# Performance work log

Hardware: AMD Instinct MI355X
Metric: run time of the kernel (lower is better)

## Reference

```python
import jax, jax.numpy as jnp
import numpy as np

B, S, D, H, F = 2, 2048, 1024, 16, 4096
HD = D // H
EPS = 1e-5


def _layernorm(x, g, b):
    mu = jnp.mean(x, axis=-1, keepdims=True)
    var = jnp.var(x, axis=-1, keepdims=True)
    return (x - mu) * jax.lax.rsqrt(var + EPS) * g + b


def setup_inputs() -> dict:
    key = jax.random.key(0)
    ks = jax.random.split(key, 10)
    sd = 0.02
    return {
        "src": jax.random.normal(ks[0], (B, S, D), jnp.float32),
        "qkv_w": jax.random.normal(ks[1], (3 * D, D), jnp.float32) * sd,
        "qkv_b": jnp.zeros((3 * D,), jnp.float32),
        "out_w": jax.random.normal(ks[2], (D, D), jnp.float32) * sd,
        "out_b": jnp.zeros((D,), jnp.float32),
        "ffn_w1": jax.random.normal(ks[3], (F, D), jnp.float32) * sd,
        "ffn_b1": jnp.zeros((F,), jnp.float32),
        "ffn_w2": jax.random.normal(ks[4], (D, F), jnp.float32) * sd,
        "ffn_b2": jnp.zeros((D,), jnp.float32),
        "ln1_g": jnp.ones((D,), jnp.float32),
        "ln1_b": jnp.zeros((D,), jnp.float32),
        "ln2_g": jnp.ones((D,), jnp.float32),
        "ln2_b": jnp.zeros((D,), jnp.float32),
    }


def reference(src, qkv_w, qkv_b, out_w, out_b, ffn_w1, ffn_b1, ffn_w2, ffn_b2,
              ln1_g, ln1_b, ln2_g, ln2_b):
    # --- Multi-head self-attention (post-norm, dropout=identity in eval) ---
    qkv = src @ qkv_w.T + qkv_b                        # [B,S,3D]
    qkv = qkv.reshape(B, S, H, 3 * HD).transpose(0, 2, 1, 3)  # [B,H,S,3hd]
    q, k, v = jnp.split(qkv, 3, axis=-1)               # each [B,H,S,hd]
    scores = jnp.einsum('bhqd,bhkd->bhqk', q, k) / np.sqrt(HD).astype(np.float32)
    attn = jax.nn.softmax(scores, axis=-1)
    ctx = jnp.einsum('bhqk,bhkd->bhqd', attn, v)       # [B,H,S,hd]
    ctx = ctx.transpose(0, 2, 1, 3).reshape(B, S, D)
    mha_out = ctx @ out_w.T + out_b
    agg = _layernorm(src + mha_out, ln1_g, ln1_b)
    # --- FFN: Linear -> ReLU -> Linear ---
    h = jax.nn.relu(agg @ ffn_w1.T + ffn_b1)
    ffn_out = h @ ffn_w2.T + ffn_b2
    return _layernorm(agg + ffn_out, ln2_g, ln2_b)
```

## Files before the change

### kernel.cpp

```cpp
#include <hip/hip_runtime.h>


typedef unsigned short u16;
typedef unsigned int u32;
typedef __attribute__((ext_vector_type(8))) __bf16 bf16x8;
typedef __attribute__((ext_vector_type(4))) float f32x4;
typedef __attribute__((ext_vector_type(4))) short s16x4;
typedef __attribute__((ext_vector_type(2))) u32 u32x2;

__device__ __forceinline__ u16 f2bf(float f) {
  u32 u = __float_as_uint(f);
  u += 0x7fffu + ((u >> 16) & 1u);
  return (u16)(u >> 16);
}

__device__ __forceinline__ float bf2f(u16 h) {
  return __uint_as_float((u32)h << 16);
}

__device__ __forceinline__ u32 pk_bf_trunc(float a, float b) {
  return (__float_as_uint(a) >> 16) | (__float_as_uint(b) & 0xffff0000u);
}

__device__ __forceinline__ float exp2_fast(float x) {
  float t = __builtin_fmaf(x, 8388608.0f, 1064992506.0f);
  return __int_as_float((int)t);
}

__device__ __forceinline__ void async16(const void* g, void* l) {
  __builtin_amdgcn_global_load_lds((__attribute__((address_space(1))) void*)g,
                                   (__attribute__((address_space(3))) void*)l,
                                   16, 0, 0);
}

__device__ __forceinline__ f32x4 mfma16(bf16x8 a, bf16x8 b, f32x4 c) {
  return __builtin_amdgcn_mfma_f32_16x16x32_bf16(a, b, c, 0, 0, 0);
}

__device__ __forceinline__ f32x4 mfma_pv(s16x4 a, s16x4 b, f32x4 c) {
#if __has_builtin(__builtin_amdgcn_mfma_f32_16x16x16bf16_1k)
  return __builtin_amdgcn_mfma_f32_16x16x16bf16_1k(a, b, c, 0, 0, 0);
#else
  f32x4 d;
  asm("v_mfma_f32_16x16x16_bf16 %0, %1, %2, %3" : "=v"(d) : "v"(a), "v"(b), "v"(c));
  return d;
#endif
}

__global__ __launch_bounds__(256)
void cvt_all(const float* __restrict__ qkv_w, const float* __restrict__ out_w,
             const float* __restrict__ f1, const float* __restrict__ f2,
             const float* __restrict__ src,
             u16* __restrict__ o_qkv, u16* __restrict__ o_out,
             u16* __restrict__ o_f1, u16* __restrict__ o_f2,
             u16* __restrict__ o_src) {
  int b = blockIdx.x;
  const float* in;
  u16* out;
  int lb, ob;
  if (b < 3072) {
    int h = b / 192, c = b - h * 192;
    ob = (c < 64) ? h * 64 + c : (c < 128) ? 1024 + h * 64 + (c - 64)
                                           : 2048 + h * 64 + (c - 128);
    in = qkv_w; out = o_qkv; lb = b;
  }
  else if (b < 4096)  { in = out_w; out = o_out; lb = b - 3072;  ob = lb; }
  else if (b < 8192)  { in = f1;    out = o_f1;  lb = b - 4096;  ob = lb; }
  else if (b < 12288) { in = f2;    out = o_f2;  lb = b - 8192;  ob = lb; }
  else                { in = src;   out = o_src; lb = b - 12288; ob = lb; }
  int i = lb * 256 + threadIdx.x;
  int o = ob * 256 + threadIdx.x;
  float4 v = ((const float4*)in)[i];
  ushort4 ov;
  ov.x = f2bf(v.x); ov.y = f2bf(v.y); ov.z = f2bf(v.z); ov.w = f2bf(v.w);
  ((ushort4*)out)[o] = ov;
}

template <int MODE, int SPLIT>
__global__ __launch_bounds__(256)
void gemm_bt(const u16* __restrict__ A, const u16* __restrict__ W,
             const float* __restrict__ bias,
             u16* __restrict__ outb,
             u16* __restrict__ qo, u16* __restrict__ ko, u16* __restrict__ vto,
             int M, int N, int K) {
  __shared__ u16 As[128 * 64];
  __shared__ u16 Bs[128 * 64];
  const int lane = threadIdx.x & 63;
  const int wave = threadIdx.x >> 6;
  const int lrow = lane & 15;
  const int lq = lane >> 4;
  const int tm = blockIdx.x * 128;
  const int tn = blockIdx.y * 128;
  const int wm = (wave >> 1) * 64;
  const int wn = (wave & 1) * 64;
  const int kc = K / SPLIT;
  const int kbeg = blockIdx.z * kc;
  f32x4 acc[4][4] = {};

  for (int k0 = kbeg; k0 < kbeg + kc; k0 += 64) {
#pragma unroll
    for (int c = 0; c < 4; ++c) {
      int chunk = wave * 256 + c * 64 + lane;
      int row = chunk >> 3;
      int sc = chunk & 7;
      int cc = sc ^ (row & 7);
      u16* la = As + (size_t)(wave * 256 + c * 64) * 8;
      u16* lb = Bs + (size_t)(wave * 256 + c * 64) * 8;
      async16(A + (size_t)(tm + row) * K + (k0 + cc * 8), la);
      async16(W + (size_t)(tn + row) * K + (k0 + cc * 8), lb);
    }
    __syncthreads();
#pragma unroll
    for (int h = 0; h < 2; ++h) {
      bf16x8 a_frag[4], b_frag[4];
#pragma unroll
      for (int i = 0; i < 4; ++i) {
        int row = wm + i * 16 + lrow;
        int sc = (h * 4 + lq) ^ (row & 7);
        a_frag[i] = *(const bf16x8*)(As + row * 64 + sc * 8);
      }
#pragma unroll
      for (int j = 0; j < 4; ++j) {
        int row = wn + j * 16 + lrow;
        int sc = (h * 4 + lq) ^ (row & 7);
        b_frag[j] = *(const bf16x8*)(Bs + row * 64 + sc * 8);
      }
#pragma unroll
      for (int i = 0; i < 4; ++i)
#pragma unroll
        for (int j = 0; j < 4; ++j)
          acc[i][j] = mfma16(a_frag[i], b_frag[j], acc[i][j]);
    }
    __syncthreads();
  }

  if constexpr (MODE == 2) {
    const int type = tn >> 10;
    if (type < 2) {
      u16* dst = (type == 0) ? qo : ko;
      const float scale = (type == 0) ? 0.1803368801f : 1.f;
#pragma unroll
      for (int j = 0; j < 4; ++j) {
        int idx = (tn & 1023) + wn + j * 16 + lrow;
        int hh = idx >> 6, c = idx & 63;
        float bv = bias[hh * 192 + type * 64 + c];
#pragma unroll
        for (int i = 0; i < 4; ++i) {
#pragma unroll
          for (int r = 0; r < 4; ++r) {
            int row = tm + wm + i * 16 + lq * 4 + r;
            int b = row >> 11, s = row & 2047;
            dst[(((size_t)(b * 16 + hh) * 2048 + s) << 6) + c] =
                f2bf((acc[i][j][r] + bv) * scale);
          }
        }
      }
    } else {
#pragma unroll
      for (int j = 0; j < 4; ++j) {
        int idx = (tn & 1023) + wn + j * 16 + lrow;
        int hh = idx >> 6, c = idx & 63;
        float bv = bias[hh * 192 + 128 + c];
#pragma unroll
        for (int i = 0; i < 4; ++i) {
          int row0 = tm + wm + i * 16 + lq * 4;
          int b = row0 >> 11, s0 = row0 & 2047;
          ushort4 pk;
          pk.x = f2bf(acc[i][j][0] + bv);
          pk.y = f2bf(acc[i][j][1] + bv);
          pk.z = f2bf(acc[i][j][2] + bv);
          pk.w = f2bf(acc[i][j][3] + bv);
          *(ushort4*)(vto + (((size_t)(b * 16 + hh) * 64 + c) << 11) + s0) = pk;
        }
      }
    }
    return;
  }

  u16* outp = outb;
  if constexpr (MODE == 0) outp += (size_t)blockIdx.z * M * N;

#pragma unroll
  for (int i = 0; i < 4; ++i) {
#pragma unroll
    for (int j = 0; j < 4; ++j) {
      int col = tn + wn + j * 16 + lrow;
      float bv = (SPLIT == 1 || blockIdx.z == 0) ? bias[col] : 0.f;
#pragma unroll
      for (int r = 0; r < 4; ++r) {
        int row = tm + wm + i * 16 + lq * 4 + r;
        float v = acc[i][j][r] + bv;
        if constexpr (MODE == 0) {
          outp[(size_t)row * N + col] = f2bf(v);
        } else {
          outp[(size_t)row * N + col] = f2bf(fmaxf(v, 0.f));
        }
      }
    }
  }
}

__global__ __launch_bounds__(512)
void attn_kernel(const u16* __restrict__ Q, const u16* __restrict__ K,
                 const u16* __restrict__ Vt,
                 u16* __restrict__ o_part, float* __restrict__ l_part) {
  __shared__ u16 Ks[128 * 64];
  __shared__ u16 Vs[64 * 128];
  const int tid = threadIdx.x;
  const int lane = tid & 63;
  const int wave = tid >> 6;
  const int wq = wave & 3;
  const int role = wave >> 2;
  const int lrow = lane & 15;
  const int q = lane >> 4;
  const int bh = blockIdx.x & 31;
  const int qb = (blockIdx.x >> 5) & 7;
  const int kvh = blockIdx.x >> 8;
  const u16* Qp = Q + ((size_t)bh * 2048 + qb * 256) * 64;
  const u16* Kp = K + (size_t)bh * 2048 * 64;
  const u16* Vp = Vt + (size_t)bh * 64 * 2048;

  bf16x8 qf[2][2];
#pragma unroll
  for (int h2 = 0; h2 < 2; ++h2)
#pragma unroll
    for (int kk = 0; kk < 2; ++kk)
      qf[h2][kk] = *(const bf16x8*)(Qp + (h2 * 128 + wave * 16 + lrow) * 64 +
                                    kk * 32 + q * 8);

  const s16x4 ones = {(short)0x3F80, (short)0x3F80, (short)0x3F80, (short)0x3F80};
  f32x4 oacc[2][4] = {};
  f32x4 lacc[2] = {};

  for (int kb = kvh * 8; kb < kvh * 8 + 8; ++kb) {
    if (role == 0) {
#pragma unroll
      for (int t = 0; t < 4; ++t) {
        int c = wq * 256 + t * 64 + lane;
        int row = c >> 3, sc = c & 7;
        int cc = sc ^ (row & 7);
        async16(Kp + (size_t)(kb * 128 + row) * 64 + cc * 8,
                Ks + (size_t)(wq * 256 + t * 64) * 8);
      }
    } else {
#pragma unroll
      for (int t = 0; t < 4; ++t) {
        int c = wq * 256 + t * 64 + lane;
        int row = c >> 4, sc = c & 15;
        int cc = sc ^ (row & 7);
        async16(Vp + (size_t)row * 2048 + kb * 128 + cc * 8,
                Vs + (size_t)(wq * 256 + t * 64) * 8);
      }
    }
    __syncthreads();

#pragma unroll
    for (int h2 = 0; h2 < 2; ++h2) {
      f32x4 sacc[8] = {};
#pragma unroll
      for (int j = 0; j < 8; ++j) {
#pragma unroll
        for (int kk = 0; kk < 2; ++kk) {
          int row = j * 16 + lrow;
          int sc = (kk * 4 + q) ^ (row & 7);
          bf16x8 kf = *(const bf16x8*)(Ks + row * 64 + sc * 8);
          sacc[j] = mfma16(kf, qf[h2][kk], sacc[j]);
        }
      }

      s16x4 pa[8];
#pragma unroll
      for (int j = 0; j < 8; ++j) {
        float p0 = exp2_fast(sacc[j][0]);
        float p1 = exp2_fast(sacc[j][1]);
        float p2 = exp2_fast(sacc[j][2]);
        float p3 = exp2_fast(sacc[j][3]);
        u32x2 pw;
        pw.x = pk_bf_trunc(p0, p1);
        pw.y = pk_bf_trunc(p2, p3);
        pa[j] = __builtin_bit_cast(s16x4, pw);
      }

#pragma unroll
      for (int j = 0; j < 8; ++j) {
        lacc[h2] = mfma_pv(pa[j], ones, lacc[h2]);
#pragma unroll
        for (int jn = 0; jn < 4; ++jn) {
          int row = jn * 16 + lrow;
          int sc = (j * 2 + (q >> 1)) ^ (row & 7);
          s16x4 vb = *(const s16x4*)(Vs + row * 128 + sc * 8 + (q & 1) * 4);
          oacc[h2][jn] = mfma_pv(pa[j], vb, oacc[h2][jn]);
        }
      }
    }
    __syncthreads();
  }

  const int b = bh >> 4, h = bh & 15;
  u16* op = o_part + (size_t)kvh * 4096 * 1024;
  float* lp = l_part + kvh * 65536 + bh * 2048;
#pragma unroll
  for (int h2 = 0; h2 < 2; ++h2) {
#pragma unroll
    for (int r = 0; r < 4; ++r) {
      int s = qb * 256 + h2 * 128 + wave * 16 + q * 4 + r;
      if (lrow == 0) lp[s] = lacc[h2][r];
      size_t base = ((size_t)(b * 2048 + s)) * 1024 + h * 64;
#pragma unroll
      for (int jn = 0; jn < 4; ++jn)
        op[base + jn * 16 + lrow] = f2bf(oacc[h2][jn][r]);
    }
  }
}

__global__ __launch_bounds__(256)
void attn_combine(const u16* __restrict__ o_part, const float* __restrict__ l_part,
                  u16* __restrict__ ctx) {
  const int t = blockIdx.x;
  const int tid = threadIdx.x;
  __shared__ float linv[16];
  if (tid < 16) {
    int b = t >> 11, s = t & 2047;
    int bh = b * 16 + tid;
    linv[tid] = 1.f / (l_part[bh * 2048 + s] + l_part[65536 + bh * 2048 + s]);
  }
  __syncthreads();
  size_t base = (size_t)t * 1024;
  ushort4 a = ((const ushort4*)(o_part + base))[tid];
  ushort4 c = ((const ushort4*)(o_part + 4096ull * 1024 + base))[tid];
  float li = linv[tid >> 4];
  ushort4 o;
  o.x = f2bf((bf2f(a.x) + bf2f(c.x)) * li);
  o.y = f2bf((bf2f(a.y) + bf2f(c.y)) * li);
  o.z = f2bf((bf2f(a.z) + bf2f(c.z)) * li);
  o.w = f2bf((bf2f(a.w) + bf2f(c.w)) * li);
  ((ushort4*)(ctx + base))[tid] = o;
}

template <int P>
__global__ __launch_bounds__(256)
void ln_kernel(const float* __restrict__ x1, const u16* __restrict__ x2,
               const float* __restrict__ g, const float* __restrict__ bb,
               float* __restrict__ outf, u16* __restrict__ outb) {
  const int t = blockIdx.x;
  const int tid = threadIdx.x;
  const int lane = tid & 63, wave = tid >> 6;
  const size_t base = (size_t)t * 1024;
  const size_t pstride = 4096ull * 1024;
  float v[4];
  float s = 0.f, s2 = 0.f;
#pragma unroll
  for (int e = 0; e < 4; ++e) {
    int i = tid + e * 256;
    float x = x1[base + i];
#pragma unroll
    for (int p = 0; p < P; ++p) x += bf2f(x2[p * pstride + base + i]);
    v[e] = x;
    s += x;
    s2 += x * x;
  }
#pragma unroll
  for (int d = 1; d < 64; d <<= 1) {
    s += __shfl_xor(s, d);
    s2 += __shfl_xor(s2, d);
  }
  __shared__ float red[8];
  if (lane == 0) { red[wave] = s; red[4 + wave] = s2; }
  __syncthreads();
  s = red[0] + red[1] + red[2] + red[3];
  s2 = red[4] + red[5] + red[6] + red[7];
  float mean = s * (1.f / 1024.f);
  float var = s2 * (1.f / 1024.f) - mean * mean;
  float rstd = rsqrtf(var + 1e-5f);
#pragma unroll
  for (int e = 0; e < 4; ++e) {
    int i = tid + e * 256;
    float y = (v[e] - mean) * rstd * g[i] + bb[i];
    outf[base + i] = y;
    if (outb) outb[base + i] = f2bf(y);
  }
}

extern "C" void kernel_launch(void* const* d_in, const int* in_sizes, int n_in,
                              void* d_out, int out_size, void* d_ws, size_t ws_size,
                              hipStream_t stream) {
  const float* src    = (const float*)d_in[0];
  const float* qkv_w  = (const float*)d_in[1];
  const float* qkv_b  = (const float*)d_in[2];
  const float* out_w  = (const float*)d_in[3];
  const float* out_b  = (const float*)d_in[4];
  const float* ffn_w1 = (const float*)d_in[5];
  const float* ffn_b1 = (const float*)d_in[6];
  const float* ffn_w2 = (const float*)d_in[7];
  const float* ffn_b2 = (const float*)d_in[8];
  const float* ln1_g  = (const float*)d_in[9];
  const float* ln1_b  = (const float*)d_in[10];
  const float* ln2_g  = (const float*)d_in[11];
  const float* ln2_b  = (const float*)d_in[12];

  char* ws = (char*)d_ws;
  size_t off = 0;
  auto alloc = [&](size_t bytes) -> void* {
    void* p = ws + off;
    off += (bytes + 255) & ~(size_t)255;
    return p;
  };
  u16* wqkv = (u16*)alloc(3072ull * 1024 * 2);
  u16* wout = (u16*)alloc(1024ull * 1024 * 2);
  u16* wf1  = (u16*)alloc(4096ull * 1024 * 2);
  u16* wf2  = (u16*)alloc(1024ull * 4096 * 2);
  u16* srcb = (u16*)alloc(4096ull * 1024 * 2);
  u16* qb_  = (u16*)alloc(32ull * 2048 * 64 * 2);
  u16* kb_  = (u16*)alloc(32ull * 2048 * 64 * 2);
  u16* vtb  = (u16*)alloc(32ull * 64 * 2048 * 2);
  u16* opart = (u16*)alloc(2ull * 4096 * 1024 * 2);
  float* lpart = (float*)alloc(2ull * 65536 * 4);
  u16* ctxb = (u16*)alloc(4096ull * 1024 * 2);
  u16* mha  = (u16*)alloc(4ull * 4096 * 1024 * 2);
  float* aggf = (float*)alloc(4096ull * 1024 * 4);
  u16* aggb = (u16*)alloc(4096ull * 1024 * 2);
  u16* hb   = (u16*)alloc(4096ull * 4096 * 2);
  u16* ffnf = (u16*)alloc(4ull * 4096 * 1024 * 2);

  cvt_all<<<16384, 256, 0, stream>>>(qkv_w, out_w, ffn_w1, ffn_w2, src,
                                     wqkv, wout, wf1, wf2, srcb);

  gemm_bt<2, 1><<<dim3(32, 24), 256, 0, stream>>>(srcb, wqkv, qkv_b, nullptr,
                                                  qb_, kb_, vtb, 4096, 3072, 1024);
  attn_kernel<<<512, 512, 0, stream>>>(qb_, kb_, vtb, opart, lpart);
  attn_combine<<<4096, 256, 0, stream>>>(opart, lpart, ctxb);
  gemm_bt<0, 4><<<dim3(32, 8, 4), 256, 0, stream>>>(ctxb, wout, out_b, mha,
                                                    nullptr, nullptr, nullptr, 4096, 1024, 1024);
  ln_kernel<4><<<4096, 256, 0, stream>>>(src, mha, ln1_g, ln1_b, aggf, aggb);
  gemm_bt<1, 1><<<dim3(32, 32), 256, 0, stream>>>(aggb, wf1, ffn_b1, hb,
                                                  nullptr, nullptr, nullptr, 4096, 4096, 1024);
  gemm_bt<0, 4><<<dim3(32, 8, 4), 256, 0, stream>>>(hb, wf2, ffn_b2, ffnf,
                                                    nullptr, nullptr, nullptr, 4096, 1024, 4096);
  ln_kernel<4><<<4096, 256, 0, stream>>>(aggf, ffnf, ln2_g, ln2_b, (float*)d_out, nullptr);
}
```

Baseline: 382.8 us.

## Add 256x256-tile 8-wave ping-pong GEMM for QKV and FFN1 projections

Adds a new GEMM kernel with 256x256 output tiles, 8 waves, and 128KB dynamic LDS holding double-buffered A/B tiles. Its main loop interleaves async global-to-LDS staging with quarter-tile MFMA phases under barriers and s_setprio, so loads overlap compute. The QKV projection (with its head-split Q/K/V^T epilogue moved over) and the FFN1 ReLU GEMM now use it with XCD-aware block swizzling, replacing the 128x128 kernel. The trade-off is high register and LDS pressure with few workgroups: 192 and 256 blocks respectively.

Result: faster. 374.7 us (-2.1%).

```diff
diff --git a/kernel.cpp b/kernel.cpp
--- a/kernel.cpp
+++ b/kernel.cpp
@@ -134,49 +134,6 @@
     __syncthreads();
   }
 
-  if constexpr (MODE == 2) {
-    const int type = tn >> 10;
-    if (type < 2) {
-      u16* dst = (type == 0) ? qo : ko;
-      const float scale = (type == 0) ? 0.1803368801f : 1.f;
-#pragma unroll
-      for (int j = 0; j < 4; ++j) {
-        int idx = (tn & 1023) + wn + j * 16 + lrow;
-        int hh = idx >> 6, c = idx & 63;
-        float bv = bias[hh * 192 + type * 64 + c];
-#pragma unroll
-        for (int i = 0; i < 4; ++i) {
-#pragma unroll
-          for (int r = 0; r < 4; ++r) {
-            int row = tm + wm + i * 16 + lq * 4 + r;
-            int b = row >> 11, s = row & 2047;
-            dst[(((size_t)(b * 16 + hh) * 2048 + s) << 6) + c] =
-                f2bf((acc[i][j][r] + bv) * scale);
-          }
-        }
-      }
-    } else {
-#pragma unroll
-      for (int j = 0; j < 4; ++j) {
-        int idx = (tn & 1023) + wn + j * 16 + lrow;
-        int hh = idx >> 6, c = idx & 63;
-        float bv = bias[hh * 192 + 128 + c];
-#pragma unroll
-        for (int i = 0; i < 4; ++i) {
-          int row0 = tm + wm + i * 16 + lq * 4;
-          int b = row0 >> 11, s0 = row0 & 2047;
-          ushort4 pk;
-          pk.x = f2bf(acc[i][j][0] + bv);
-          pk.y = f2bf(acc[i][j][1] + bv);
-          pk.z = f2bf(acc[i][j][2] + bv);
-          pk.w = f2bf(acc[i][j][3] + bv);
-          *(ushort4*)(vto + (((size_t)(b * 16 + hh) * 64 + c) << 11) + s0) = pk;
-        }
-      }
-    }
-    return;
-  }
-
   u16* outp = outb;
   if constexpr (MODE == 0) outp += (size_t)blockIdx.z * M * N;
 
@@ -194,6 +151,257 @@
           outp[(size_t)row * N + col] = f2bf(v);
         } else {
           outp[(size_t)row * N + col] = f2bf(fmaxf(v, 0.f));
+        }
+      }
+    }
+  }
+}
+
+template <int MODE>
+__global__ __launch_bounds__(512, 2)
+void gemm8p(const u16* __restrict__ A, const u16* __restrict__ W,
+            const float* __restrict__ bias, u16* __restrict__ outb,
+            u16* __restrict__ qo, u16* __restrict__ ko, u16* __restrict__ vto,
+            int N) {
+  extern __shared__ u16 lds[];
+  constexpr int K = 1024;
+  constexpr int NTK = K / 64;
+  constexpr int NG = NTK / 2;
+  u16* As = lds;
+  u16* Bs = lds + 32768;
+  const int tid = threadIdx.x;
+  const int lane = tid & 63;
+  const int wave = tid >> 6;
+  const int lrow = lane & 15;
+  const int lq = lane >> 4;
+  const int wm = wave >> 2;
+  const int wn = wave & 3;
+
+  const int nwg = gridDim.x;
+  const int wg = blockIdx.x;
+  const int swz = (wg & 7) * (nwg >> 3) + (wg >> 3);
+  const int tm = (swz & 15) * 256;
+  const int tn = (swz >> 4) * 256;
+
+  auto stage = [&](const u16* __restrict__ T, int trow0, int kt, int rbase,
+                   u16* base) {
+#pragma unroll
+    for (int it = 0; it < 2; ++it) {
+      int c = it * 512 + tid;
+      int row = c >> 3, sc = c & 7, cc = sc ^ (row & 7);
+      async16(T + (size_t)(trow0 + rbase + row) * K + kt * 64 + cc * 8,
+              base + rbase * 64 + (it * 512 + wave * 64) * 8);
+    }
+  };
+  auto ldA = [&](int buf, int m, int h) {
+    int row = wm * 128 + m * 16 + lrow;
+    int sc = (h * 4 + lq) ^ (row & 7);
+    return *(const bf16x8*)(As + buf * 16384 + row * 64 + sc * 8);
+  };
+  auto ldB = [&](int buf, int n, int h) {
+    int row = wn * 64 + n * 16 + lrow;
+    int sc = (h * 4 + lq) ^ (row & 7);
+    return *(const bf16x8*)(Bs + buf * 16384 + row * 64 + sc * 8);
+  };
+
+  f32x4 acc[8][4] = {};
+  bf16x8 a[4][2], b[4][2];
+
+  stage(A, tm, 0, 0, As);
+  stage(A, tm, 0, 128, As);
+  stage(W, tn, 0, 0, Bs);
+  stage(W, tn, 0, 128, Bs);
+  stage(W, tn, 1, 0, Bs + 16384);
+  stage(A, tm, 1, 0, As + 16384);
+  asm volatile("s_waitcnt vmcnt(4)" ::: "memory");
+  __builtin_amdgcn_s_barrier();
+
+  for (int g = 0; g < NG; ++g) {
+    const int t = 2 * g;
+    const int t1k = t + 1;
+    const int t2k = (t + 2 < NTK) ? t + 2 : NTK - 1;
+    const int t3k = (t + 3 < NTK) ? t + 3 : NTK - 1;
+
+#pragma unroll
+    for (int m = 0; m < 4; ++m) { a[m][0] = ldA(0, m, 0); a[m][1] = ldA(0, m, 1); }
+#pragma unroll
+    for (int n = 0; n < 2; ++n) { b[n][0] = ldB(0, n, 0); b[n][1] = ldB(0, n, 1); }
+    stage(A, tm, t1k, 128, As + 16384);
+    __builtin_amdgcn_s_barrier();
+    asm volatile("s_waitcnt lgkmcnt(0)" ::: "memory");
+    __builtin_amdgcn_s_setprio(1);
+#pragma unroll
+    for (int m = 0; m < 4; ++m)
+#pragma unroll
+      for (int n = 0; n < 2; ++n) {
+        acc[m][n] = mfma16(a[m][0], b[n][0], acc[m][n]);
+        acc[m][n] = mfma16(a[m][1], b[n][1], acc[m][n]);
+      }
+    __builtin_amdgcn_s_setprio(0);
+    __builtin_amdgcn_s_barrier();
+
+#pragma unroll
+    for (int n = 0; n < 2; ++n) { b[2 + n][0] = ldB(0, 2 + n, 0); b[2 + n][1] = ldB(0, 2 + n, 1); }
+    stage(W, tn, t1k, 128, Bs + 16384);
+    __builtin_amdgcn_s_barrier();
+    asm volatile("s_waitcnt lgkmcnt(0)" ::: "memory");
+    __builtin_amdgcn_s_setprio(1);
+#pragma unroll
+    for (int m = 0; m < 4; ++m)
+#pragma unroll
+      for (int n = 0; n < 2; ++n) {
+        acc[m][2 + n] = mfma16(a[m][0], b[2 + n][0], acc[m][2 + n]);
+        acc[m][2 + n] = mfma16(a[m][1], b[2 + n][1], acc[m][2 + n]);
+      }
+    __builtin_amdgcn_s_setprio(0);
+    __builtin_amdgcn_s_barrier();
+
+#pragma unroll
+    for (int m = 0; m < 4; ++m) { a[m][0] = ldA(0, 4 + m, 0); a[m][1] = ldA(0, 4 + m, 1); }
+    stage(W, tn, t2k, 0, Bs);
+    __builtin_amdgcn_s_barrier();
+    asm volatile("s_waitcnt lgkmcnt(0)" ::: "memory");
+    __builtin_amdgcn_s_setprio(1);
+#pragma unroll
+    for (int m = 0; m < 4; ++m)
+#pragma unroll
+      for (int n = 0; n < 2; ++n) {
+        acc[4 + m][n] = mfma16(a[m][0], b[n][0], acc[4 + m][n]);
+        acc[4 + m][n] = mfma16(a[m][1], b[n][1], acc[4 + m][n]);
+      }
+    __builtin_amdgcn_s_setprio(0);
+    __builtin_amdgcn_s_barrier();
+
+    stage(A, tm, t2k, 0, As);
+    asm volatile("s_waitcnt vmcnt(4)" ::: "memory");
+    __builtin_amdgcn_s_barrier();
+    __builtin_amdgcn_s_setprio(1);
+#pragma unroll
+    for (int m = 0; m < 4; ++m)
+#pragma unroll
+      for (int n = 0; n < 2; ++n) {
+        acc[4 + m][2 + n] = mfma16(a[m][0], b[2 + n][0], acc[4 + m][2 + n]);
+        acc[4 + m][2 + n] = mfma16(a[m][1], b[2 + n][1], acc[4 + m][2 + n]);
+      }
+    __builtin_amdgcn_s_setprio(0);
+    __builtin_amdgcn_s_barrier();
+
+#pragma unroll
+    for (int m = 0; m < 4; ++m) { a[m][0] = ldA(1, m, 0); a[m][1] = ldA(1, m, 1); }
+#pragma unroll
+    for (int n = 0; n < 2; ++n) { b[n][0] = ldB(1, n, 0); b[n][1] = ldB(1, n, 1); }
+    stage(A, tm, t2k, 128, As);
+    __builtin_amdgcn_s_barrier();
+    asm volatile("s_waitcnt lgkmcnt(0)" ::: "memory");
+    __builtin_amdgcn_s_setprio(1);
+#pragma unroll
+    for (int m = 0; m < 4; ++m)
+#pragma unroll
+      for (int n = 0; n < 2; ++n) {
+        acc[m][n] = mfma16(a[m][0], b[n][0], acc[m][n]);
+        acc[m][n] = mfma16(a[m][1], b[n][1], acc[m][n]);
+      }
+    __builtin_amdgcn_s_setprio(0);
+    __builtin_amdgcn_s_barrier();
+
+#pragma unroll
+    for (int n = 0; n < 2; ++n) { b[2 + n][0] = ldB(1, 2 + n, 0); b[2 + n][1] = ldB(1, 2 + n, 1); }
+    stage(W, tn, t2k, 128, Bs);
+    __builtin_amdgcn_s_barrier();
+    asm volatile("s_waitcnt lgkmcnt(0)" ::: "memory");
+    __builtin_amdgcn_s_setprio(1);
+#pragma unroll
+    for (int m = 0; m < 4; ++m)
+#pragma unroll
+      for (int n = 0; n < 2; ++n) {
+        acc[m][2 + n] = mfma16(a[m][0], b[2 + n][0], acc[m][2 + n]);
+        acc[m][2 + n] = mfma16(a[m][1], b[2 + n][1], acc[m][2 + n]);
+      }
+    __builtin_amdgcn_s_setprio(0);
+    __builtin_amdgcn_s_barrier();
+
+#pragma unroll
+    for (int m = 0; m < 4; ++m) { a[m][0] = ldA(1, 4 + m, 0); a[m][1] = ldA(1, 4 + m, 1); }
+    stage(W, tn, t3k, 0, Bs + 16384);
+    __builtin_amdgcn_s_barrier();
+    asm volatile("s_waitcnt lgkmcnt(0)" ::: "memory");
+    __builtin_amdgcn_s_setprio(1);
+#pragma unroll
+    for (int m = 0; m < 4; ++m)
+#pragma unroll
+      for (int n = 0; n < 2; ++n) {
+        acc[4 + m][n] = mfma16(a[m][0], b[n][0], acc[4 + m][n]);
+        acc[4 + m][n] = mfma16(a[m][1], b[n][1], acc[4 + m][n]);
+      }
+    __builtin_amdgcn_s_setprio(0);
+    __builtin_amdgcn_s_barrier();
+
+    stage(A, tm, t3k, 0, As + 16384);
+    asm volatile("s_waitcnt vmcnt(4)" ::: "memory");
+    __builtin_amdgcn_s_barrier();
+    __builtin_amdgcn_s_setprio(1);
+#pragma unroll
+    for (int m = 0; m < 4; ++m)
+#pragma unroll
+      for (int n = 0; n < 2; ++n) {
+        acc[4 + m][2 + n] = mfma16(a[m][0], b[2 + n][0], acc[4 + m][2 + n]);
+        acc[4 + m][2 + n] = mfma16(a[m][1], b[2 + n][1], acc[4 + m][2 + n]);
+      }
+    __builtin_amdgcn_s_setprio(0);
+    __builtin_amdgcn_s_barrier();
+  }
+  asm volatile("s_waitcnt vmcnt(0)" ::: "memory");
+
+  if constexpr (MODE == 1) {
+#pragma unroll
+    for (int m = 0; m < 8; ++m)
+#pragma unroll
+      for (int n = 0; n < 4; ++n) {
+        int col = tn + wn * 64 + n * 16 + lrow;
+        float bv = bias[col];
+#pragma unroll
+        for (int r = 0; r < 4; ++r) {
+          int row = tm + wm * 128 + m * 16 + lq * 4 + r;
+          outb[(size_t)row * N + col] = f2bf(fmaxf(acc[m][n][r] + bv, 0.f));
+        }
+      }
+  } else {
+    const int type = tn >> 10;
+    if (type < 2) {
+      u16* dst = (type == 0) ? qo : ko;
+      const float scale = (type == 0) ? 0.1803368801f : 1.f;
+#pragma unroll
+      for (int n = 0; n < 4; ++n) {
+        int idx = (tn & 1023) + wn * 64 + n * 16 + lrow;
+        int hh = idx >> 6, c = idx & 63;
+        float bv = bias[hh * 192 + type * 64 + c];
+#pragma unroll
+        for (int m = 0; m < 8; ++m) {
+#pragma unroll
+          for (int r = 0; r < 4; ++r) {
+            int row = tm + wm * 128 + m * 16 + lq * 4 + r;
+            int bb = row >> 11, s = row & 2047;
+            dst[(((size_t)(bb * 16 + hh) * 2048 + s) << 6) + c] =
+                f2bf((acc[m][n][r] + bv) * scale);
+          }
+        }
+      }
+    } else {
+#pragma unroll
+      for (int n = 0; n < 4; ++n) {
+        int idx = (tn & 1023) + wn * 64 + n * 16 + lrow;
+        int hh = idx >> 6, c = idx & 63;
+        float bv = bias[hh * 192 + 128 + c];
+#pragma unroll
+        for (int m = 0; m < 8; ++m) {
+          int row0 = tm + wm * 128 + m * 16 + lq * 4;
+          int bb = row0 >> 11, s0 = row0 & 2047;
+          ushort4 pk;
+          pk.x = f2bf(acc[m][n][0] + bv);
+          pk.y = f2bf(acc[m][n][1] + bv);
+          pk.z = f2bf(acc[m][n][2] + bv);
+          pk.w = f2bf(acc[m][n][3] + bv);
+          *(ushort4*)(vto + (((size_t)(bb * 16 + hh) * 64 + c) << 11) + s0) = pk;
         }
       }
     }
@@ -422,18 +630,29 @@
   u16* hb   = (u16*)alloc(4096ull * 4096 * 2);
   u16* ffnf = (u16*)alloc(4ull * 4096 * 1024 * 2);
 
+  static bool attr_done = false;
+  if (!attr_done) {
+    auto* kq = gemm8p<2>;
+    auto* kf = gemm8p<1>;
+    hipFuncSetAttribute(reinterpret_cast<const void*>(kq),
+                        hipFuncAttributeMaxDynamicSharedMemorySize, 131072);
+    hipFuncSetAttribute(reinterpret_cast<const void*>(kf),
+                        hipFuncAttributeMaxDynamicSharedMemorySize, 131072);
+    attr_done = true;
+  }
+
   cvt_all<<<16384, 256, 0, stream>>>(qkv_w, out_w, ffn_w1, ffn_w2, src,
                                      wqkv, wout, wf1, wf2, srcb);
 
-  gemm_bt<2, 1><<<dim3(32, 24), 256, 0, stream>>>(srcb, wqkv, qkv_b, nullptr,
-                                                  qb_, kb_, vtb, 4096, 3072, 1024);
+  gemm8p<2><<<192, 512, 131072, stream>>>(srcb, wqkv, qkv_b, nullptr,
+                                          qb_, kb_, vtb, 3072);
   attn_kernel<<<512, 512, 0, stream>>>(qb_, kb_, vtb, opart, lpart);
   attn_combine<<<4096, 256, 0, stream>>>(opart, lpart, ctxb);
   gemm_bt<0, 4><<<dim3(32, 8, 4), 256, 0, stream>>>(ctxb, wout, out_b, mha,
                                                     nullptr, nullptr, nullptr, 4096, 1024, 1024);
   ln_kernel<4><<<4096, 256, 0, stream>>>(src, mha, ln1_g, ln1_b, aggf, aggb);
-  gemm_bt<1, 1><<<dim3(32, 32), 256, 0, stream>>>(aggb, wf1, ffn_b1, hb,
-                                                  nullptr, nullptr, nullptr, 4096, 4096, 1024);
+  gemm8p<1><<<256, 512, 131072, stream>>>(aggb, wf1, ffn_b1, hb,
+                                          nullptr, nullptr, nullptr, 4096);
   gemm_bt<0, 4><<<dim3(32, 8, 4), 256, 0, stream>>>(hb, wf2, ffn_b2, ffnf,
                                                     nullptr, nullptr, nullptr, 4096, 1024, 4096);
   ln_kernel<4><<<4096, 256, 0, stream>>>(aggf, ffnf, ln2_g, ln2_b, (float*)d_out, nullptr);
```
